# Optimization experiments

Hardware: AMD Instinct MI355X
Metric: run time of the kernel (lower is better)

The kernel has to match this reference:

```python
import jax, jax.numpy as jnp
import numpy as np

N, E, F, H1, H2, D1, P = 50000, 400000, 256, 128, 128, 512, 100000


def setup_inputs() -> dict:
    key = jax.random.key(0)
    keys = iter(jax.random.split(key, 40))
    def glorot(shape):
        lim = float(np.sqrt(6.0 / (shape[0] + shape[1])))
        return jax.random.uniform(next(keys), shape, jnp.float32, -lim, lim)
    inp = {}
    inp["x_o"] = jax.random.normal(next(keys), (N, F), jnp.float32)
    inp["x_a"] = jax.random.normal(next(keys), (N, F), jnp.float32)
    inp["edge_index_o"] = jax.random.randint(next(keys), (2, E), 0, N)
    inp["edge_index_s"] = jax.random.randint(next(keys), (2, E), 0, N)
    inp["idx"] = jax.random.randint(next(keys), (2, P), 0, N)
    def gin_params(cin, cout, name):
        inp["eps_" + name] = jnp.zeros(())  # train_eps init = 0
        inp["w1_" + name] = glorot((cin, 2 * cout))
        inp["b1_" + name] = jnp.zeros((2 * cout,))
        inp["w2_" + name] = glorot((2 * cout, cout))
        inp["b2_" + name] = jnp.zeros((cout,))
    gin_params(F, H1, "o1"); gin_params(F, H1, "s1")
    gin_params(2 * H1, H2, "o2"); gin_params(2 * H1, H2, "s2")
    inp["disc_w"] = glorot((2 * H2, 2 * H2))  # nn.Bilinear(n_h, n_h, 1) weight, xavier
    inp["disc_b"] = jnp.zeros((1,))
    inp["dec1_w"] = glorot((8 * H2, D1))
    inp["dec1_b"] = jnp.zeros((D1,))
    inp["dec2_w"] = glorot((D1, 1))
    inp["dec2_b"] = jnp.zeros((1,))
    return inp


def reference(x_o, x_a, edge_index_o, edge_index_s, idx,
              eps_o1, w1_o1, b1_o1, w2_o1, b2_o1,
              eps_s1, w1_s1, b1_s1, w2_s1, b2_s1,
              eps_o2, w1_o2, b1_o2, w2_o2, b2_o2,
              eps_s2, w1_s2, b1_s2, w2_s2, b2_s2,
              disc_w, disc_b, dec1_w, dec1_b, dec2_w, dec2_b):
    def gin(x, ei, eps, w1, b1, w2, b2):
        # GINConv: mlp((1+eps)*x + sum_{j->i} x_j); MLP = Linear->relu->Linear
        agg = jax.ops.segment_sum(x[ei[0]], ei[1], num_segments=x.shape[0])
        h = (1.0 + eps) * x + agg
        return jax.nn.relu(h @ w1 + b1) @ w2 + b2

    def encode(x):
        x1o = jax.nn.relu(gin(x, edge_index_o, eps_o1, w1_o1, b1_o1, w2_o1, b2_o1))
        x1s = jax.nn.relu(gin(x, edge_index_s, eps_s1, w1_s1, b1_s1, w2_s1, b2_s1))
        x1 = jnp.concatenate([x1o, x1s], axis=1)  # dropout: eval mode -> identity
        x2o = gin(x1, edge_index_o, eps_o2, w1_o2, b1_o2, w2_o2, b2_o2)
        x2s = gin(x1, edge_index_s, eps_s2, w1_s2, b1_s2, w2_s2, b2_s2)
        return jnp.concatenate([x2o, x2s], axis=1)  # [N, 2*H2]

    x2_os = encode(x_o)
    x2_os_a = encode(x_a)

    h_os = jax.nn.sigmoid(jnp.mean(x2_os, axis=0))      # AvgReadout + sigmoid, [2*H2]
    h_os_a = jax.nn.sigmoid(jnp.mean(x2_os_a, axis=0))

    def disc(c, h_pl, h_mi):
        # Bilinear(n_h, n_h, 1): sc[n] = sum_ij h[n,i] W[i,j] c[j] + b
        v = disc_w @ c                       # [2*H2]
        sc1 = h_pl @ v + disc_b              # [N]
        sc2 = h_mi @ v + disc_b
        return jnp.stack([sc1, sc2], axis=1)  # [N, 2]

    ret_os = disc(h_os, x2_os, x2_os_a)
    ret_os_a = disc(h_os_a, x2_os_a, x2_os)

    e1 = x2_os[idx[0]]                       # [P, 2*H2]
    e2 = x2_os[idx[1]]
    feat = jnp.concatenate([e1 + e2, e1 * e2, e1, e2], axis=1)  # [P, 8*H2]
    log = jax.nn.relu(feat @ dec1_w + dec1_b) @ dec2_w + dec2_b  # [P, 1]
    return (log, ret_os, ret_os_a, x2_os)
```

## Files before the change

kernel.cpp:

```cpp
#include <hip/hip_runtime.h>
#include <hip/hip_bf16.h>
#include <stdint.h>

#define N_NODES 50000
#define N_EDGES 400000
#define FDIM    256
#define PPAIRS  100000

typedef float f4 __attribute__((ext_vector_type(4)));
typedef float f2 __attribute__((ext_vector_type(2)));
typedef short s8v __attribute__((ext_vector_type(8)));
typedef float f32x4 __attribute__((ext_vector_type(4)));
typedef unsigned short u16;

__device__ inline u16 f2bf(float v) {
    union { float f; uint32_t u; } x; x.f = v;
    uint32_t r = x.u + 0x7fffu + ((x.u >> 16) & 1u);
    return (u16)(r >> 16);
}
__device__ inline float bf2f(u16 b) {
    union { uint32_t u; float f; } x; x.u = ((uint32_t)b) << 16;
    return x.f;
}
__device__ inline f32x4 mfma16(s8v a, s8v b, f32x4 c) {
    return __builtin_amdgcn_mfma_f32_16x16x32_bf16(a, b, c, 0, 0, 0);
}

__global__ void count_deg(const int* __restrict__ dst, int* __restrict__ deg, int e) {
    int t = blockIdx.x * blockDim.x + threadIdx.x;
    if (t < e) atomicAdd(&deg[dst[t]], 1);
}

__global__ void exclusive_scan(const int* __restrict__ deg, int* __restrict__ rowptr, int n) {
    __shared__ int sums[1024];
    int t = threadIdx.x;
    int chunk = (n + 1023) >> 10;
    int begin = t * chunk;
    int end   = min(begin + chunk, n);
    int s = 0;
    for (int i = begin; i < end; ++i) s += deg[i];
    sums[t] = s;
    __syncthreads();
    for (int off = 1; off < 1024; off <<= 1) {
        int v = (t >= off) ? sums[t - off] : 0;
        __syncthreads();
        sums[t] += v;
        __syncthreads();
    }
    int prefix = (t == 0) ? 0 : sums[t - 1];
    for (int i = begin; i < end; ++i) { rowptr[i] = prefix; prefix += deg[i]; }
    if (t == 1023) rowptr[n] = sums[1023];
}

__global__ void fill_csr(const int* __restrict__ src, const int* __restrict__ dst,
                         const int* __restrict__ rowptr, int* __restrict__ cursor,
                         int* __restrict__ col, int e) {
    int t = blockIdx.x * blockDim.x + threadIdx.x;
    if (t < e) {
        int d = dst[t];
        int pos = atomicAdd(&cursor[d], 1);
        col[rowptr[d] + pos] = src[t];
    }
}

__global__ __launch_bounds__(256) void agg_h_split(
        const float* __restrict__ x, const int* __restrict__ rowptr,
        const int* __restrict__ col, const float* __restrict__ eps,
        u16* __restrict__ hh, u16* __restrict__ hl, int n) {
    int gw = (blockIdx.x * 256 + threadIdx.x) >> 6;
    int l  = threadIdx.x & 63;
    if (gw >= n) return;
    float e = 1.0f + eps[0];
    f4 acc = {0.f, 0.f, 0.f, 0.f};
    int b0 = rowptr[gw], b1 = rowptr[gw + 1];
    for (int i = b0; i < b1; ++i) {
        int s = col[i];
        acc += *(const f4*)&x[(size_t)s * FDIM + 4 * l];
    }
    f4 self = *(const f4*)&x[(size_t)gw * FDIM + 4 * l];
    f4 r = e * self + acc;
    u16 hb[4], lb[4];
#pragma unroll
    for (int c = 0; c < 4; ++c) {
        hb[c] = f2bf(r[c]);
        lb[c] = f2bf(r[c] - bf2f(hb[c]));
    }
    uint2 hv, lv;
    hv.x = (uint32_t)hb[0] | ((uint32_t)hb[1] << 16);
    hv.y = (uint32_t)hb[2] | ((uint32_t)hb[3] << 16);
    lv.x = (uint32_t)lb[0] | ((uint32_t)lb[1] << 16);
    lv.y = (uint32_t)lb[2] | ((uint32_t)lb[3] << 16);
    *(uint2*)&hh[(size_t)gw * FDIM + 4 * l] = hv;
    *(uint2*)&hl[(size_t)gw * FDIM + 4 * l] = lv;
}

__global__ void split_w(const float* __restrict__ W, u16* __restrict__ Wh,
                        u16* __restrict__ Wl, int K, int Nc) {
    int t = blockIdx.x * 256 + threadIdx.x;
    if (t >= K * Nc) return;
    int k = t / Nc, c = t - k * Nc;
    float v = W[t];
    u16 h = f2bf(v);
    u16 lo = f2bf(v - bf2f(h));
    int dst = ((k >> 3) * Nc + c) * 8 + (k & 7);
    Wh[dst] = h; Wl[dst] = lo;
}

__global__ void prep_decw(const float* __restrict__ w1, u16* __restrict__ Wh,
                          u16* __restrict__ Wl) {
    int t = blockIdx.x * 256 + threadIdx.x;
    if (t >= 768 * 512) return;
    int k = t >> 9, c = t & 511;
    float v;
    if (k < 256)       v = w1[(size_t)k * 512 + c] + w1[(size_t)(512 + k) * 512 + c];
    else if (k < 512)  v = w1[(size_t)(k - 256) * 512 + c] + w1[(size_t)(768 + k - 256) * 512 + c];
    else               v = w1[(size_t)(256 + k - 512) * 512 + c];
    u16 h = f2bf(v);
    u16 lo = f2bf(v - bf2f(h));
    int dst = ((k >> 3) * 512 + c) * 8 + (k & 7);
    Wh[dst] = h; Wl[dst] = lo;
}

template <int EPI, bool RELU>
__global__ __launch_bounds__(512) void mfma_gemm(
        const u16* __restrict__ Ah, const u16* __restrict__ Al,
        const u16* __restrict__ Bh, const u16* __restrict__ Bl,
        const float* __restrict__ bias,
        u16* __restrict__ Ch, u16* __restrict__ Cl,
        float* __restrict__ Cf, int ldc, int coloff,
        int n, int nout) {
    __shared__ __align__(16) u16 As[2][2][4][128][8];
    __shared__ __align__(16) u16 Bs[2][2][4][128][8];
    int t = threadIdx.x;
    int w = t >> 6, lm = t & 15, lg = (t >> 4) & 3;
    int row0 = blockIdx.x * 128;
    int c0   = blockIdx.y * 128;
    int srow = t & 127, skg = (t >> 7) & 3;

    int garow = min(row0 + srow, n - 1);
    const u16* gAh = Ah + (size_t)garow * 256 + skg * 8;
    const u16* gAl = Al + (size_t)garow * 256 + skg * 8;
    const u16* gBh = Bh + ((size_t)skg * nout + c0 + srow) * 8;
    const u16* gBl = Bl + ((size_t)skg * nout + c0 + srow) * 8;
    const size_t bstep = (size_t)4 * nout * 8;

    f32x4 acc[8] = {};
    uint4 rAh, rAl, rBh, rBl;

    rAh = *(const uint4*)(gAh);
    rAl = *(const uint4*)(gAl);
    rBh = *(const uint4*)(gBh);
    rBl = *(const uint4*)(gBl);
    *(uint4*)&As[0][0][skg][srow][0] = rAh;
    *(uint4*)&As[0][1][skg][srow][0] = rAl;
    *(uint4*)&Bs[0][0][skg][srow][0] = rBh;
    *(uint4*)&Bs[0][1][skg][srow][0] = rBl;
    __syncthreads();

    int cur = 0;
#pragma unroll
    for (int c = 0; c < 8; ++c) {
        if (c < 7) {
            rAh = *(const uint4*)(gAh + (c + 1) * 32);
            rAl = *(const uint4*)(gAl + (c + 1) * 32);
            rBh = *(const uint4*)(gBh + (c + 1) * bstep);
            rBl = *(const uint4*)(gBl + (c + 1) * bstep);
        }
        s8v bh = *(const s8v*)&Bs[cur][0][lg][w * 16 + lm][0];
        s8v bl = *(const s8v*)&Bs[cur][1][lg][w * 16 + lm][0];
#pragma unroll
        for (int R = 0; R < 8; R += 2) {
            s8v ah0 = *(const s8v*)&As[cur][0][lg][R * 16 + lm][0];
            s8v al0 = *(const s8v*)&As[cur][1][lg][R * 16 + lm][0];
            s8v ah1 = *(const s8v*)&As[cur][0][lg][(R + 1) * 16 + lm][0];
            s8v al1 = *(const s8v*)&As[cur][1][lg][(R + 1) * 16 + lm][0];
            acc[R]     = mfma16(ah0, bh, acc[R]);
            acc[R + 1] = mfma16(ah1, bh, acc[R + 1]);
            acc[R]     = mfma16(ah0, bl, acc[R]);
            acc[R + 1] = mfma16(ah1, bl, acc[R + 1]);
            acc[R]     = mfma16(al0, bh, acc[R]);
            acc[R + 1] = mfma16(al1, bh, acc[R + 1]);
        }
        if (c < 7) {
            int nb = cur ^ 1;
            *(uint4*)&As[nb][0][skg][srow][0] = rAh;
            *(uint4*)&As[nb][1][skg][srow][0] = rAl;
            *(uint4*)&Bs[nb][0][skg][srow][0] = rBh;
            *(uint4*)&Bs[nb][1][skg][srow][0] = rBl;
        }
        __syncthreads();
        cur ^= 1;
    }

    int cg = c0 + w * 16 + lm;
    float bv = bias[cg];
#pragma unroll
    for (int R = 0; R < 8; ++R) {
#pragma unroll
        for (int i = 0; i < 4; ++i) {
            int r = row0 + R * 16 + lg * 4 + i;
            if (r < n) {
                float v = acc[R][i] + bv;
                if (RELU) v = fmaxf(v, 0.f);
                if (EPI == 0) {
                    u16 hbv = f2bf(v);
                    Ch[(size_t)r * 256 + cg] = hbv;
                    Cl[(size_t)r * 256 + cg] = f2bf(v - bf2f(hbv));
                } else {
                    Cf[(size_t)r * ldc + coloff + cg] = v;
                }
            }
        }
    }
}

__global__ __launch_bounds__(512) void decoder_mfma(
        const float* __restrict__ x2os, const int* __restrict__ idx0,
        const int* __restrict__ idx1,
        const u16* __restrict__ Wh, const u16* __restrict__ Wl,
        const float* __restrict__ b1, const float* __restrict__ w2,
        float* __restrict__ partial) {
    __shared__ __align__(16) u16 As[2][2][4][128][8];
    __shared__ __align__(16) u16 Bs[2][2][4][128][8];
    int t = threadIdx.x;
    int w = t >> 6, lm = t & 15, lg = (t >> 4) & 3;
    int p0 = blockIdx.x * 128;
    int c0 = blockIdx.y * 128;
    int srow = t & 127, skg = (t >> 7) & 3;

    int p = min(p0 + srow, PPAIRS - 1);
    int n1 = idx0[p], n2 = idx1[p];
    const float* e1p = x2os + (size_t)n1 * 256;
    const float* e2p = x2os + (size_t)n2 * 256;
    const u16* gBh = Wh + ((size_t)skg * 512 + c0 + srow) * 8;
    const u16* gBl = Wl + ((size_t)skg * 512 + c0 + srow) * 8;
    const size_t bstep = (size_t)4 * 512 * 8;

    f32x4 acc[8] = {};
    f4 r1a, r1b, r2a, r2b;
    uint4 rBh, rBl;

    auto loadA = [&](int c) {
        int kb = c * 32;
        int reg = kb >> 8;
        int fb = (kb & 255) + skg * 8;
        if (reg == 0)      { r1a = *(const f4*)(e1p + fb); r1b = *(const f4*)(e1p + fb + 4); }
        else if (reg == 1) { r1a = *(const f4*)(e2p + fb); r1b = *(const f4*)(e2p + fb + 4); }
        else {               r1a = *(const f4*)(e1p + fb); r1b = *(const f4*)(e1p + fb + 4);
                             r2a = *(const f4*)(e2p + fb); r2b = *(const f4*)(e2p + fb + 4); }
    };
    auto writeA = [&](int nb, int c) {
        int reg = (c * 32) >> 8;
        float v[8];
#pragma unroll
        for (int q = 0; q < 4; ++q) { v[q] = r1a[q]; v[4 + q] = r1b[q]; }
        if (reg == 2) {
#pragma unroll
            for (int q = 0; q < 4; ++q) { v[q] *= r2a[q]; v[4 + q] *= r2b[q]; }
        }
        u16 hb[8], lb[8];
#pragma unroll
        for (int q = 0; q < 8; ++q) { hb[q] = f2bf(v[q]); lb[q] = f2bf(v[q] - bf2f(hb[q])); }
        uint4 hv, lv;
        hv.x = (uint32_t)hb[0] | ((uint32_t)hb[1] << 16);
        hv.y = (uint32_t)hb[2] | ((uint32_t)hb[3] << 16);
        hv.z = (uint32_t)hb[4] | ((uint32_t)hb[5] << 16);
        hv.w = (uint32_t)hb[6] | ((uint32_t)hb[7] << 16);
        lv.x = (uint32_t)lb[0] | ((uint32_t)lb[1] << 16);
        lv.y = (uint32_t)lb[2] | ((uint32_t)lb[3] << 16);
        lv.z = (uint32_t)lb[4] | ((uint32_t)lb[5] << 16);
        lv.w = (uint32_t)lb[6] | ((uint32_t)lb[7] << 16);
        *(uint4*)&As[nb][0][skg][srow][0] = hv;
        *(uint4*)&As[nb][1][skg][srow][0] = lv;
    };

    loadA(0);
    rBh = *(const uint4*)(gBh);
    rBl = *(const uint4*)(gBl);
    writeA(0, 0);
    *(uint4*)&Bs[0][0][skg][srow][0] = rBh;
    *(uint4*)&Bs[0][1][skg][srow][0] = rBl;
    __syncthreads();

    int cur = 0;
#pragma unroll
    for (int c = 0; c < 24; ++c) {
        if (c < 23) {
            loadA(c + 1);
            rBh = *(const uint4*)(gBh + (c + 1) * bstep);
            rBl = *(const uint4*)(gBl + (c + 1) * bstep);
        }
        s8v bh = *(const s8v*)&Bs[cur][0][lg][w * 16 + lm][0];
        s8v bl = *(const s8v*)&Bs[cur][1][lg][w * 16 + lm][0];
#pragma unroll
        for (int R = 0; R < 8; R += 2) {
            s8v ah0 = *(const s8v*)&As[cur][0][lg][R * 16 + lm][0];
            s8v al0 = *(const s8v*)&As[cur][1][lg][R * 16 + lm][0];
            s8v ah1 = *(const s8v*)&As[cur][0][lg][(R + 1) * 16 + lm][0];
            s8v al1 = *(const s8v*)&As[cur][1][lg][(R + 1) * 16 + lm][0];
            acc[R]     = mfma16(ah0, bh, acc[R]);
            acc[R + 1] = mfma16(ah1, bh, acc[R + 1]);
            acc[R]     = mfma16(ah0, bl, acc[R]);
            acc[R + 1] = mfma16(ah1, bl, acc[R + 1]);
            acc[R]     = mfma16(al0, bh, acc[R]);
            acc[R + 1] = mfma16(al1, bh, acc[R + 1]);
        }
        if (c < 23) {
            int nb = cur ^ 1;
            writeA(nb, c + 1);
            *(uint4*)&Bs[nb][0][skg][srow][0] = rBh;
            *(uint4*)&Bs[nb][1][skg][srow][0] = rBl;
        }
        __syncthreads();
        cur ^= 1;
    }

    int cg = c0 + w * 16 + lm;
    float bv = b1[cg], w2v = w2[cg];
    int cb = blockIdx.y;
#pragma unroll
    for (int R = 0; R < 8; ++R) {
#pragma unroll
        for (int i = 0; i < 4; ++i) {
            float v = fmaxf(acc[R][i] + bv, 0.f) * w2v;
            v += __shfl_xor(v, 1);
            v += __shfl_xor(v, 2);
            v += __shfl_xor(v, 4);
            v += __shfl_xor(v, 8);
            if (lm == 0) {
                int pr = p0 + R * 16 + lg * 4 + i;
                if (pr < PPAIRS) partial[(size_t)pr * 32 + cb * 8 + w] = v;
            }
        }
    }
}

__global__ void finalize_out(const float* __restrict__ partial,
                             const float* __restrict__ b2, float* __restrict__ out) {
    int p = blockIdx.x * 256 + threadIdx.x;
    if (p < PPAIRS) {
        float s = 0.f;
#pragma unroll
        for (int q = 0; q < 8; ++q) {
            f4 v = *(const f4*)&partial[(size_t)p * 32 + q * 4];
            s += v[0] + v[1] + v[2] + v[3];
        }
        out[p] = s + b2[0];
    }
}

__global__ void colsum(const float* __restrict__ x, float* __restrict__ mean_out, int n) {
    int rows = (n + gridDim.x - 1) / gridDim.x;
    int r0 = blockIdx.x * rows;
    int r1 = min(r0 + rows, n);
    float s = 0.f;
    for (int r = r0; r < r1; ++r) s += x[(size_t)r * FDIM + threadIdx.x];
    atomicAdd(&mean_out[threadIdx.x], s);
}

__global__ void disc_prep(const float* __restrict__ means, const float* __restrict__ disc_w,
                          float* __restrict__ vv, float invn) {
    __shared__ float c0[256], c1[256];
    int t = threadIdx.x;
    c0[t] = 1.f / (1.f + expf(-means[t] * invn));
    c1[t] = 1.f / (1.f + expf(-means[256 + t] * invn));
    __syncthreads();
    float v0 = 0.f, v1 = 0.f;
    for (int j = 0; j < 256; ++j) {
        float wv = disc_w[t * 256 + j];
        v0 += wv * c0[j];
        v1 += wv * c1[j];
    }
    vv[t] = v0;
    vv[256 + t] = v1;
}

__global__ __launch_bounds__(256) void disc_score(
        const float* __restrict__ x2os, const float* __restrict__ x2a,
        const float* __restrict__ vv, const float* __restrict__ disc_b,
        float* __restrict__ ret_os, float* __restrict__ ret_osa, int n) {
    int gw = (blockIdx.x * 256 + threadIdx.x) >> 6;
    int l  = threadIdx.x & 63;
    if (gw >= n) return;
    f4 a  = *(const f4*)&x2os[(size_t)gw * FDIM + 4 * l];
    f4 b  = *(const f4*)&x2a[(size_t)gw * FDIM + 4 * l];
    f4 v0 = *(const f4*)&vv[4 * l];
    f4 v1 = *(const f4*)&vv[256 + 4 * l];
    float d1 = a[0]*v0[0] + a[1]*v0[1] + a[2]*v0[2] + a[3]*v0[3];
    float d2 = b[0]*v0[0] + b[1]*v0[1] + b[2]*v0[2] + b[3]*v0[3];
    float d3 = b[0]*v1[0] + b[1]*v1[1] + b[2]*v1[2] + b[3]*v1[3];
    float d4 = a[0]*v1[0] + a[1]*v1[1] + a[2]*v1[2] + a[3]*v1[3];
    for (int off = 32; off > 0; off >>= 1) {
        d1 += __shfl_down(d1, off);
        d2 += __shfl_down(d2, off);
        d3 += __shfl_down(d3, off);
        d4 += __shfl_down(d4, off);
    }
    if (l == 0) {
        float db = disc_b[0];
        ret_os[2 * gw]      = d1 + db;
        ret_os[2 * gw + 1]  = d2 + db;
        ret_osa[2 * gw]     = d3 + db;
        ret_osa[2 * gw + 1] = d4 + db;
    }
}

extern "C" void kernel_launch(void* const* d_in, const int* in_sizes, int n_in,
                              void* d_out, int out_size, void* d_ws, size_t ws_size,
                              hipStream_t stream) {
    const float* x_o   = (const float*)d_in[0];
    const float* x_a   = (const float*)d_in[1];
    const int*   ei_o  = (const int*)d_in[2];
    const int*   ei_s  = (const int*)d_in[3];
    const int*   idx   = (const int*)d_in[4];
    const float* eps_o1 = (const float*)d_in[5];
    const float* w1_o1 = (const float*)d_in[6];
    const float* b1_o1 = (const float*)d_in[7];
    const float* w2_o1 = (const float*)d_in[8];
    const float* b2_o1 = (const float*)d_in[9];
    const float* eps_s1 = (const float*)d_in[10];
    const float* w1_s1 = (const float*)d_in[11];
    const float* b1_s1 = (const float*)d_in[12];
    const float* w2_s1 = (const float*)d_in[13];
    const float* b2_s1 = (const float*)d_in[14];
    const float* eps_o2 = (const float*)d_in[15];
    const float* w1_o2 = (const float*)d_in[16];
    const float* b1_o2 = (const float*)d_in[17];
    const float* w2_o2 = (const float*)d_in[18];
    const float* b2_o2 = (const float*)d_in[19];
    const float* eps_s2 = (const float*)d_in[20];
    const float* w1_s2 = (const float*)d_in[21];
    const float* b1_s2 = (const float*)d_in[22];
    const float* w2_s2 = (const float*)d_in[23];
    const float* b2_s2 = (const float*)d_in[24];
    const float* disc_w = (const float*)d_in[25];
    const float* disc_b = (const float*)d_in[26];
    const float* dec1_w = (const float*)d_in[27];
    const float* dec1_b = (const float*)d_in[28];
    const float* dec2_w = (const float*)d_in[29];
    const float* dec2_b = (const float*)d_in[30];

    float* out_log = (float*)d_out;
    float* ret_os  = out_log + PPAIRS;
    float* ret_osa = ret_os + 2 * N_NODES;
    float* x2_os   = ret_osa + 2 * N_NODES;

    char* wp = (char*)d_ws;
    auto alloc = [&](size_t bytes) -> void* {
        void* p = (void*)wp;
        wp += (bytes + 255) & ~(size_t)255;
        return p;
    };
    int*   rowptr_o = (int*)alloc((N_NODES + 1) * sizeof(int));
    int*   rowptr_s = (int*)alloc((N_NODES + 1) * sizeof(int));
    int*   col_o    = (int*)alloc((size_t)N_EDGES * sizeof(int));
    int*   col_s    = (int*)alloc((size_t)N_EDGES * sizeof(int));
    int*   cursor   = (int*)alloc((size_t)N_NODES * sizeof(int));
    u16*   hh       = (u16*)alloc((size_t)N_NODES * FDIM * 2);
    u16*   hl       = (u16*)alloc((size_t)N_NODES * FDIM * 2);
    u16*   th       = (u16*)alloc((size_t)N_NODES * FDIM * 2);
    u16*   tl       = (u16*)alloc((size_t)N_NODES * FDIM * 2);
    float* x1buf    = (float*)alloc((size_t)N_NODES * FDIM * sizeof(float));
    float* x2a      = (float*)alloc((size_t)N_NODES * FDIM * sizeof(float));
    float* partial  = (float*)alloc((size_t)PPAIRS * 32 * sizeof(float));
    float* means    = (float*)alloc(512 * sizeof(float));
    float* vv       = (float*)alloc(512 * sizeof(float));
    u16* w1h[4]; u16* w1l[4]; u16* w2h[4]; u16* w2l[4];
    for (int i = 0; i < 4; ++i) {
        w1h[i] = (u16*)alloc(256 * 256 * 2); w1l[i] = (u16*)alloc(256 * 256 * 2);
        w2h[i] = (u16*)alloc(256 * 128 * 2); w2l[i] = (u16*)alloc(256 * 128 * 2);
    }
    u16* decWh = (u16*)alloc(768 * 512 * 2);
    u16* decWl = (u16*)alloc(768 * 512 * 2);

    const int EB = (N_EDGES + 255) / 256;
    hipMemsetAsync(means, 0, 512 * sizeof(float), stream);

    hipMemsetAsync(cursor, 0, N_NODES * sizeof(int), stream);
    count_deg<<<EB, 256, 0, stream>>>(ei_o + N_EDGES, cursor, N_EDGES);
    exclusive_scan<<<1, 1024, 0, stream>>>(cursor, rowptr_o, N_NODES);
    hipMemsetAsync(cursor, 0, N_NODES * sizeof(int), stream);
    fill_csr<<<EB, 256, 0, stream>>>(ei_o, ei_o + N_EDGES, rowptr_o, cursor, col_o, N_EDGES);
    hipMemsetAsync(cursor, 0, N_NODES * sizeof(int), stream);
    count_deg<<<EB, 256, 0, stream>>>(ei_s + N_EDGES, cursor, N_EDGES);
    exclusive_scan<<<1, 1024, 0, stream>>>(cursor, rowptr_s, N_NODES);
    hipMemsetAsync(cursor, 0, N_NODES * sizeof(int), stream);
    fill_csr<<<EB, 256, 0, stream>>>(ei_s, ei_s + N_EDGES, rowptr_s, cursor, col_s, N_EDGES);

    const float* w1s[4] = {w1_o1, w1_s1, w1_o2, w1_s2};
    const float* w2s[4] = {w2_o1, w2_s1, w2_o2, w2_s2};
    for (int i = 0; i < 4; ++i) {
        split_w<<<(256 * 256 + 255) / 256, 256, 0, stream>>>(w1s[i], w1h[i], w1l[i], 256, 256);
        split_w<<<(256 * 128 + 255) / 256, 256, 0, stream>>>(w2s[i], w2h[i], w2l[i], 256, 128);
    }
    prep_decw<<<(768 * 512 + 255) / 256, 256, 0, stream>>>(dec1_w, decWh, decWl);

    const int AGGB = (N_NODES + 3) / 4;
    const int RB   = (N_NODES + 127) / 128;

    auto conv = [&](const float* xin, const int* rp, const int* cl, const float* epsv,
                    int wi, const float* b1v, const float* b2v,
                    float* outbuf, int coloff, bool relu2) {
        agg_h_split<<<AGGB, 256, 0, stream>>>(xin, rp, cl, epsv, hh, hl, N_NODES);
        mfma_gemm<0, true><<<dim3(RB, 2), 512, 0, stream>>>(
            hh, hl, w1h[wi], w1l[wi], b1v, th, tl, nullptr, 0, 0, N_NODES, 256);
        if (relu2)
            mfma_gemm<1, true><<<dim3(RB, 1), 512, 0, stream>>>(
                th, tl, w2h[wi], w2l[wi], b2v, nullptr, nullptr, outbuf, 256, coloff, N_NODES, 128);
        else
            mfma_gemm<1, false><<<dim3(RB, 1), 512, 0, stream>>>(
                th, tl, w2h[wi], w2l[wi], b2v, nullptr, nullptr, outbuf, 256, coloff, N_NODES, 128);
    };

    auto encode = [&](const float* x, float* x2out) {
        conv(x,     rowptr_o, col_o, eps_o1, 0, b1_o1, b2_o1, x1buf, 0,   true);
        conv(x,     rowptr_s, col_s, eps_s1, 1, b1_s1, b2_s1, x1buf, 128, true);
        conv(x1buf, rowptr_o, col_o, eps_o2, 2, b1_o2, b2_o2, x2out, 0,   false);
        conv(x1buf, rowptr_s, col_s, eps_s2, 3, b1_s2, b2_s2, x2out, 128, false);
    };

    encode(x_o, x2_os);
    encode(x_a, x2a);

    colsum<<<128, 256, 0, stream>>>(x2_os, means, N_NODES);
    colsum<<<128, 256, 0, stream>>>(x2a, means + 256, N_NODES);
    disc_prep<<<1, 256, 0, stream>>>(means, disc_w, vv, 1.0f / (float)N_NODES);
    disc_score<<<(N_NODES + 3) / 4, 256, 0, stream>>>(x2_os, x2a, vv, disc_b,
                                                      ret_os, ret_osa, N_NODES);

    const int DB = (PPAIRS + 127) / 128;
    decoder_mfma<<<dim3(DB, 4), 512, 0, stream>>>(x2_os, idx, idx + PPAIRS,
                                                  decWh, decWl, dec1_b, dec2_w, partial);
    finalize_out<<<(PPAIRS + 255) / 256, 256, 0, stream>>>(partial, dec2_b, out_log);
}
```

Before: 2.445 ms.

## Restructure decoder to cover all 512 columns per block, unroll aggregation gather

The decoder now has each block compute all 512 hidden columns for 64 pairs. B fragments are read straight from global memory into registers instead of being staged through shared memory, which removes the 4x redundant gather and bf16 split of A across the former column grid. The partial buffer shrinks from 32 to 8 entries per pair. Separately, the GIN aggregation loop is unrolled 4x with independent accumulators to raise memory-level parallelism. Risks include higher register pressure from 16 accumulator tiles and uncoalesced or L2-bound global weight loads in the inner loop.

```diff
diff --git a/kernel.cpp b/kernel.cpp
--- a/kernel.cpp
+++ b/kernel.cpp
@@ -71,14 +71,23 @@
     int l  = threadIdx.x & 63;
     if (gw >= n) return;
     float e = 1.0f + eps[0];
-    f4 acc = {0.f, 0.f, 0.f, 0.f};
     int b0 = rowptr[gw], b1 = rowptr[gw + 1];
-    for (int i = b0; i < b1; ++i) {
+    f4 a0 = {0.f, 0.f, 0.f, 0.f}, a1 = a0, a2 = a0, a3 = a0;
+    int i = b0;
+    for (; i + 4 <= b1; i += 4) {
+        int s0 = col[i], s1 = col[i + 1], s2 = col[i + 2], s3 = col[i + 3];
+        f4 v0 = *(const f4*)&x[(size_t)s0 * FDIM + 4 * l];
+        f4 v1 = *(const f4*)&x[(size_t)s1 * FDIM + 4 * l];
+        f4 v2 = *(const f4*)&x[(size_t)s2 * FDIM + 4 * l];
+        f4 v3 = *(const f4*)&x[(size_t)s3 * FDIM + 4 * l];
+        a0 += v0; a1 += v1; a2 += v2; a3 += v3;
+    }
+    for (; i < b1; ++i) {
         int s = col[i];
-        acc += *(const f4*)&x[(size_t)s * FDIM + 4 * l];
+        a0 += *(const f4*)&x[(size_t)s * FDIM + 4 * l];
     }
     f4 self = *(const f4*)&x[(size_t)gw * FDIM + 4 * l];
-    f4 r = e * self + acc;
+    f4 r = e * self + ((a0 + a1) + (a2 + a3));
     u16 hb[4], lb[4];
 #pragma unroll
     for (int c = 0; c < 4; ++c) {
@@ -220,116 +229,97 @@
         const u16* __restrict__ Wh, const u16* __restrict__ Wl,
         const float* __restrict__ b1, const float* __restrict__ w2,
         float* __restrict__ partial) {
-    __shared__ __align__(16) u16 As[2][2][4][128][8];
-    __shared__ __align__(16) u16 Bs[2][2][4][128][8];
+    __shared__ __align__(16) u16 As[2][2][4][64][8];
     int t = threadIdx.x;
     int w = t >> 6, lm = t & 15, lg = (t >> 4) & 3;
-    int p0 = blockIdx.x * 128;
-    int c0 = blockIdx.y * 128;
-    int srow = t & 127, skg = (t >> 7) & 3;
-
+    int p0 = blockIdx.x * 64;
+
+    int slot = t >> 1, half = t & 1;
+    int srow = slot & 63, skg = slot >> 6;
     int p = min(p0 + srow, PPAIRS - 1);
     int n1 = idx0[p], n2 = idx1[p];
     const float* e1p = x2os + (size_t)n1 * 256;
     const float* e2p = x2os + (size_t)n2 * 256;
-    const u16* gBh = Wh + ((size_t)skg * 512 + c0 + srow) * 8;
-    const u16* gBl = Wl + ((size_t)skg * 512 + c0 + srow) * 8;
-    const size_t bstep = (size_t)4 * 512 * 8;
-
-    f32x4 acc[8] = {};
-    f4 r1a, r1b, r2a, r2b;
-    uint4 rBh, rBl;
+
+    f32x4 acc[4][4] = {};
+    f4 r1, r2;
 
     auto loadA = [&](int c) {
         int kb = c * 32;
         int reg = kb >> 8;
-        int fb = (kb & 255) + skg * 8;
-        if (reg == 0)      { r1a = *(const f4*)(e1p + fb); r1b = *(const f4*)(e1p + fb + 4); }
-        else if (reg == 1) { r1a = *(const f4*)(e2p + fb); r1b = *(const f4*)(e2p + fb + 4); }
-        else {               r1a = *(const f4*)(e1p + fb); r1b = *(const f4*)(e1p + fb + 4);
-                             r2a = *(const f4*)(e2p + fb); r2b = *(const f4*)(e2p + fb + 4); }
+        int fb = (kb & 255) + skg * 8 + half * 4;
+        if (reg == 0)      { r1 = *(const f4*)(e1p + fb); }
+        else if (reg == 1) { r1 = *(const f4*)(e2p + fb); }
+        else {               r1 = *(const f4*)(e1p + fb); r2 = *(const f4*)(e2p + fb); }
     };
     auto writeA = [&](int nb, int c) {
         int reg = (c * 32) >> 8;
-        float v[8];
-#pragma unroll
-        for (int q = 0; q < 4; ++q) { v[q] = r1a[q]; v[4 + q] = r1b[q]; }
-        if (reg == 2) {
-#pragma unroll
-            for (int q = 0; q < 4; ++q) { v[q] *= r2a[q]; v[4 + q] *= r2b[q]; }
-        }
-        u16 hb[8], lb[8];
-#pragma unroll
-        for (int q = 0; q < 8; ++q) { hb[q] = f2bf(v[q]); lb[q] = f2bf(v[q] - bf2f(hb[q])); }
-        uint4 hv, lv;
+        f4 v = r1;
+        if (reg == 2) v *= r2;
+        u16 hb[4], lb[4];
+#pragma unroll
+        for (int q = 0; q < 4; ++q) { hb[q] = f2bf(v[q]); lb[q] = f2bf(v[q] - bf2f(hb[q])); }
+        uint2 hv, lv;
         hv.x = (uint32_t)hb[0] | ((uint32_t)hb[1] << 16);
         hv.y = (uint32_t)hb[2] | ((uint32_t)hb[3] << 16);
-        hv.z = (uint32_t)hb[4] | ((uint32_t)hb[5] << 16);
-        hv.w = (uint32_t)hb[6] | ((uint32_t)hb[7] << 16);
         lv.x = (uint32_t)lb[0] | ((uint32_t)lb[1] << 16);
         lv.y = (uint32_t)lb[2] | ((uint32_t)lb[3] << 16);
-        lv.z = (uint32_t)lb[4] | ((uint32_t)lb[5] << 16);
-        lv.w = (uint32_t)lb[6] | ((uint32_t)lb[7] << 16);
-        *(uint4*)&As[nb][0][skg][srow][0] = hv;
-        *(uint4*)&As[nb][1][skg][srow][0] = lv;
+        *(uint2*)&As[nb][0][skg][srow][half * 4] = hv;
+        *(uint2*)&As[nb][1][skg][srow][half * 4] = lv;
     };
 
     loadA(0);
-    rBh = *(const uint4*)(gBh);
-    rBl = *(const uint4*)(gBl);
     writeA(0, 0);
-    *(uint4*)&Bs[0][0][skg][srow][0] = rBh;
-    *(uint4*)&Bs[0][1][skg][srow][0] = rBl;
     __syncthreads();
 
     int cur = 0;
-#pragma unroll
+#pragma unroll 1
     for (int c = 0; c < 24; ++c) {
-        if (c < 23) {
-            loadA(c + 1);
-            rBh = *(const uint4*)(gBh + (c + 1) * bstep);
-            rBl = *(const uint4*)(gBl + (c + 1) * bstep);
-        }
-        s8v bh = *(const s8v*)&Bs[cur][0][lg][w * 16 + lm][0];
-        s8v bl = *(const s8v*)&Bs[cur][1][lg][w * 16 + lm][0];
-#pragma unroll
-        for (int R = 0; R < 8; R += 2) {
-            s8v ah0 = *(const s8v*)&As[cur][0][lg][R * 16 + lm][0];
-            s8v al0 = *(const s8v*)&As[cur][1][lg][R * 16 + lm][0];
-            s8v ah1 = *(const s8v*)&As[cur][0][lg][(R + 1) * 16 + lm][0];
-            s8v al1 = *(const s8v*)&As[cur][1][lg][(R + 1) * 16 + lm][0];
-            acc[R]     = mfma16(ah0, bh, acc[R]);
-            acc[R + 1] = mfma16(ah1, bh, acc[R + 1]);
-            acc[R]     = mfma16(ah0, bl, acc[R]);
-            acc[R + 1] = mfma16(ah1, bl, acc[R + 1]);
-            acc[R]     = mfma16(al0, bh, acc[R]);
-            acc[R + 1] = mfma16(al1, bh, acc[R + 1]);
-        }
-        if (c < 23) {
-            int nb = cur ^ 1;
-            writeA(nb, c + 1);
-            *(uint4*)&Bs[nb][0][skg][srow][0] = rBh;
-            *(uint4*)&Bs[nb][1][skg][srow][0] = rBl;
-        }
+        if (c < 23) loadA(c + 1);
+        s8v bh[4], bl[4];
+#pragma unroll
+        for (int ct = 0; ct < 4; ++ct) {
+            size_t boff = ((size_t)(c * 4 + lg) * 512 + w * 64 + ct * 16 + lm) * 8;
+            bh[ct] = *(const s8v*)(Wh + boff);
+            bl[ct] = *(const s8v*)(Wl + boff);
+        }
+#pragma unroll
+        for (int R = 0; R < 4; ++R) {
+            s8v ah = *(const s8v*)&As[cur][0][lg][R * 16 + lm][0];
+            s8v al = *(const s8v*)&As[cur][1][lg][R * 16 + lm][0];
+#pragma unroll
+            for (int ct = 0; ct < 4; ++ct) {
+                acc[R][ct] = mfma16(ah, bh[ct], acc[R][ct]);
+                acc[R][ct] = mfma16(ah, bl[ct], acc[R][ct]);
+                acc[R][ct] = mfma16(al, bh[ct], acc[R][ct]);
+            }
+        }
+        if (c < 23) writeA(cur ^ 1, c + 1);
         __syncthreads();
         cur ^= 1;
     }
 
-    int cg = c0 + w * 16 + lm;
-    float bv = b1[cg], w2v = w2[cg];
-    int cb = blockIdx.y;
-#pragma unroll
-    for (int R = 0; R < 8; ++R) {
+    float bv[4], wv[4];
+#pragma unroll
+    for (int ct = 0; ct < 4; ++ct) {
+        int cg = w * 64 + ct * 16 + lm;
+        bv[ct] = b1[cg]; wv[ct] = w2[cg];
+    }
+#pragma unroll
+    for (int R = 0; R < 4; ++R) {
 #pragma unroll
         for (int i = 0; i < 4; ++i) {
-            float v = fmaxf(acc[R][i] + bv, 0.f) * w2v;
+            float v = 0.f;
+#pragma unroll
+            for (int ct = 0; ct < 4; ++ct)
+                v += fmaxf(acc[R][ct][i] + bv[ct], 0.f) * wv[ct];
             v += __shfl_xor(v, 1);
             v += __shfl_xor(v, 2);
             v += __shfl_xor(v, 4);
             v += __shfl_xor(v, 8);
             if (lm == 0) {
                 int pr = p0 + R * 16 + lg * 4 + i;
-                if (pr < PPAIRS) partial[(size_t)pr * 32 + cb * 8 + w] = v;
+                if (pr < PPAIRS) partial[(size_t)pr * 8 + w] = v;
             }
         }
     }
@@ -341,8 +331,8 @@
     if (p < PPAIRS) {
         float s = 0.f;
 #pragma unroll
-        for (int q = 0; q < 8; ++q) {
-            f4 v = *(const f4*)&partial[(size_t)p * 32 + q * 4];
+        for (int q = 0; q < 2; ++q) {
+            f4 v = *(const f4*)&partial[(size_t)p * 8 + q * 4];
             s += v[0] + v[1] + v[2] + v[3];
         }
         out[p] = s + b2[0];
@@ -462,7 +452,7 @@
     u16*   tl       = (u16*)alloc((size_t)N_NODES * FDIM * 2);
     float* x1buf    = (float*)alloc((size_t)N_NODES * FDIM * sizeof(float));
     float* x2a      = (float*)alloc((size_t)N_NODES * FDIM * sizeof(float));
-    float* partial  = (float*)alloc((size_t)PPAIRS * 32 * sizeof(float));
+    float* partial  = (float*)alloc((size_t)PPAIRS * 8 * sizeof(float));
     float* means    = (float*)alloc(512 * sizeof(float));
     float* vv       = (float*)alloc(512 * sizeof(float));
     u16* w1h[4]; u16* w1l[4]; u16* w2h[4]; u16* w2l[4];
@@ -528,8 +518,8 @@
     disc_score<<<(N_NODES + 3) / 4, 256, 0, stream>>>(x2_os, x2a, vv, disc_b,
                                                       ret_os, ret_osa, N_NODES);
 
-    const int DB = (PPAIRS + 127) / 128;
-    decoder_mfma<<<dim3(DB, 4), 512, 0, stream>>>(x2_os, idx, idx + PPAIRS,
-                                                  decWh, decWl, dec1_b, dec2_w, partial);
+    const int DB = (PPAIRS + 63) / 64;
+    decoder_mfma<<<DB, 512, 0, stream>>>(x2_os, idx, idx + PPAIRS,
+                                         decWh, decWl, dec1_b, dec2_w, partial);
     finalize_out<<<(PPAIRS + 255) / 256, 256, 0, stream>>>(partial, dec2_b, out_log);
 }
```

Result: faster. 2.226 ms (-8.9%).
